# Performance work log

Measured on AMD Instinct MI355X. Metric: run time of the kernel, lower is better.

Reference implementation:

```python
import jax, jax.numpy as jnp
import numpy as np

N_PILLARS_X = 512
N_PILLARS_Y = 512
IN_FEATURES = 6
OUT_FEATURES = 64
N_POINTS = 2_000_000
BN_EPS = 1e-5


def setup_inputs() -> dict:
    key = jax.random.key(0)
    k_x, k_idx, k_w, k_b, k_g, k_bt = jax.random.split(key, 6)
    x = jax.random.normal(k_x, (N_POINTS, IN_FEATURES), dtype=jnp.float32)
    indices = jax.random.randint(k_idx, (N_POINTS, 2), 0, N_PILLARS_X, dtype=jnp.int64)
    # Linear params (torch default init scale ~ 1/sqrt(fan_in))
    bound = 1.0 / np.sqrt(IN_FEATURES)
    W = jax.random.uniform(k_w, (OUT_FEATURES, IN_FEATURES), minval=-bound, maxval=bound, dtype=jnp.float32)
    b = jax.random.uniform(k_b, (OUT_FEATURES,), minval=-bound, maxval=bound, dtype=jnp.float32)
    # BatchNorm affine params (torch init: gamma=1, beta=0; perturb gamma slightly)
    gamma = jnp.ones((OUT_FEATURES,), dtype=jnp.float32)
    beta = jnp.zeros((OUT_FEATURES,), dtype=jnp.float32)
    return {"x": x, "indices": indices, "W": W, "b": b, "gamma": gamma, "beta": beta}


def reference(x, indices, W, b, gamma, beta):
    # Linear: (N, 6) @ (6, 64) + b -> (N, 64)
    h = x @ W.T + b
    # BatchNorm1d (training mode: batch statistics, biased variance)
    mean = jnp.mean(h, axis=0)
    var = jnp.mean(jnp.square(h - mean), axis=0)
    h = gamma * (h - mean) * jax.lax.rsqrt(var + BN_EPS) + beta
    h = jax.nn.relu(h)
    # Scatter-add each point's feature vector into its (x_idx, y_idx) pillar cell
    grid = jnp.zeros((N_PILLARS_X, N_PILLARS_Y, OUT_FEATURES), dtype=h.dtype)
    grid = grid.at[indices[:, 0], indices[:, 1]].add(h)
    return grid
```

## Files before the change

kernel.cpp:

```cpp
#include <hip/hip_runtime.h>
#include <hip/hip_fp16.h>


constexpr int NPTS   = 2000000;
constexpr int NBUCK  = 2048;
constexpr int CPB    = 128;
constexpr int NBLK   = 512;
constexpr int CHUNK  = (NPTS + NBLK - 1) / NBLK;
constexpr float EPS  = 1e-5f;

constexpr int WS_WPH    = 0;
constexpr int WS_BP     = 192;
constexpr int WS_BSTATS = 256;
constexpr int WS_OFFT   = WS_BSTATS + NBLK * 32;
constexpr int WS_REG    = WS_OFFT + (NBUCK + 1) * NBLK / 2;

typedef _Float16 h2v __attribute__((ext_vector_type(2)));

__device__ __forceinline__ float dot2u(unsigned int a, unsigned int b, float c) {
    union { unsigned int u; h2v h; } ca, cb;
    ca.u = a; cb.u = b;
    return __builtin_amdgcn_fdot2(ca.h, cb.h, c, false);
}

__device__ __forceinline__ float wave_sum64(float v) {
#pragma unroll
    for (int off = 32; off > 0; off >>= 1) v += __shfl_down(v, off, 64);
    return v;
}

__global__ __launch_bounds__(1024) void sort_kernel(const float* __restrict__ x,
                                                    const int2* __restrict__ idx,
                                                    unsigned short* __restrict__ offt,
                                                    uint4* __restrict__ regions,
                                                    float* __restrict__ bstats) {
    __shared__ uint4 recs[CHUNK];
    __shared__ int lh[NBUCK];
    __shared__ int wsum[16];
    __shared__ float lstats[16][27];
    const int t = threadIdx.x, lane = t & 63, wv = t >> 6;
    const int blk = blockIdx.x;
    const int ch  = ((blk & 7) << 6) | (blk >> 3);
    const int beg = ch * CHUNK, end = min(NPTS, beg + CHUNK), cnt = end - beg;

    for (int i = t; i < NBUCK; i += 1024) lh[i] = 0;
    __syncthreads();

    for (int p = beg + t; p < end; p += 1024) {
        const int2 ij = idx[p];
        atomicAdd(&lh[(ij.x << 2) | (ij.y >> 7)], 1);
    }
    __syncthreads();

    {
        const int v0 = lh[2 * t], v1 = lh[2 * t + 1];
        const int v = v0 + v1;
        int incl = v;
#pragma unroll
        for (int d = 1; d < 64; d <<= 1) {
            int u = __shfl_up(incl, d, 64);
            if (lane >= d) incl += u;
        }
        if (lane == 63) wsum[wv] = incl;
        __syncthreads();
        int pre = 0;
#pragma unroll
        for (int w = 0; w < 16; ++w) {
            int sv = wsum[w];
            if (w < wv) pre += sv;
        }
        const int excl = pre + incl - v;
        offt[(2 * t) * NBLK + ch]     = (unsigned short)excl;
        offt[(2 * t + 1) * NBLK + ch] = (unsigned short)(excl + v0);
        if (t == 1023) offt[NBUCK * NBLK + ch] = (unsigned short)(excl + v);
        lh[2 * t] = excl;
        lh[2 * t + 1] = excl + v0;
    }
    __syncthreads();

    float acc[27];
#pragma unroll
    for (int i = 0; i < 27; ++i) acc[i] = 0.f;
    for (int p = beg + t; p < end; p += 1024) {
        const int2 ij = idx[p];
        const float2* xp = (const float2*)(x + (size_t)p * 6);
        const float2 a = xp[0], bq = xp[1], cq = xp[2];
        float v[6] = {a.x, a.y, bq.x, bq.y, cq.x, cq.y};
        int c = 6;
#pragma unroll
        for (int k = 0; k < 6; ++k) {
            acc[k] += v[k];
#pragma unroll
            for (int l = k; l < 6; ++l) { acc[c] += v[k] * v[l]; ++c; }
        }
        __half2 h0 = __floats2half2_rn(a.x, a.y);
        __half2 h1 = __floats2half2_rn(bq.x, bq.y);
        __half2 h2 = __floats2half2_rn(cq.x, cq.y);
        const int b = (ij.x << 2) | (ij.y >> 7);
        const int dst = atomicAdd(&lh[b], 1);
        uint4 r;
        r.x = *(const unsigned int*)&h0;
        r.y = *(const unsigned int*)&h1;
        r.z = *(const unsigned int*)&h2;
        r.w = (unsigned int)(ij.y & 127);
        recs[dst] = r;
    }
    __syncthreads();

    uint4* reg = regions + (size_t)ch * CHUNK;
    for (int i = t; i < cnt; i += 1024) reg[i] = recs[i];

#pragma unroll
    for (int i = 0; i < 27; ++i) {
        const float s = wave_sum64(acc[i]);
        if (lane == 0) lstats[wv][i] = s;
    }
    __syncthreads();
    if (t < 32) {
        float s = 0.f;
        if (t < 27)
            for (int w = 0; w < 16; ++w) s += lstats[w][t];
        bstats[ch * 32 + t] = s;
    }
}

__global__ __launch_bounds__(1024) void bnfold_kernel(const float* __restrict__ bstats,
                                                      const float* __restrict__ W,
                                                      const float* __restrict__ b,
                                                      const float* __restrict__ gamma,
                                                      const float* __restrict__ beta,
                                                      float* __restrict__ ws) {
    __shared__ float lred[32][33];
    __shared__ float s27[27];
    __shared__ float m[6], C[36];
    const int t = threadIdx.x;
    {
        const int s = t & 31, seg = t >> 5;
        float a = 0.f;
#pragma unroll 4
        for (int j = 0; j < NBLK / 32; ++j) a += bstats[(seg * (NBLK / 32) + j) * 32 + s];
        lred[seg][s] = a;
    }
    __syncthreads();
    if (t < 27) {
        float s = 0.f;
#pragma unroll
        for (int g = 0; g < 32; ++g) s += lred[g][t];
        s27[t] = s;
    }
    __syncthreads();
    if (t == 0) {
        const float invN = 1.0f / (float)NPTS;
        float mm[6];
        for (int k = 0; k < 6; ++k) { mm[k] = s27[k] * invN; m[k] = mm[k]; }
        int c = 6;
        for (int k = 0; k < 6; ++k)
            for (int l = k; l < 6; ++l) {
                const float cov = s27[c] * invN - mm[k] * mm[l];
                ++c;
                C[k * 6 + l] = cov;
                C[l * 6 + k] = cov;
            }
    }
    __syncthreads();
    if (t < 64) {
        float w[6];
#pragma unroll
        for (int k = 0; k < 6; ++k) w[k] = W[t * 6 + k];
        float mh = b[t];
#pragma unroll
        for (int k = 0; k < 6; ++k) mh += w[k] * m[k];
        float var = 0.f;
#pragma unroll
        for (int k = 0; k < 6; ++k)
#pragma unroll
            for (int l = 0; l < 6; ++l) var += w[k] * w[l] * C[k * 6 + l];
        const float s = gamma[t] * rsqrtf(var + EPS);
        float wp[6];
#pragma unroll
        for (int k = 0; k < 6; ++k) wp[k] = w[k] * s;
        unsigned int* wsu = (unsigned int*)ws;
        __half2 p0 = __floats2half2_rn(wp[0], wp[1]);
        __half2 p1 = __floats2half2_rn(wp[2], wp[3]);
        __half2 p2 = __floats2half2_rn(wp[4], wp[5]);
        wsu[WS_WPH + t * 3 + 0] = *(const unsigned int*)&p0;
        wsu[WS_WPH + t * 3 + 1] = *(const unsigned int*)&p1;
        wsu[WS_WPH + t * 3 + 2] = *(const unsigned int*)&p2;
        ws[WS_BP + t] = beta[t] + s * (b[t] - mh);
    }
}

constexpr int CAP   = 1152;
constexpr int OVCAP = 16;
constexpr int ACCT  = 256;
constexpr int RPT   = (CAP + ACCT - 1) / ACCT;

__global__ __launch_bounds__(ACCT, 8) void accum_kernel(const uint4* __restrict__ regions,
                                                        const unsigned int* __restrict__ offt32,
                                                        const float* __restrict__ wsf,
                                                        float* __restrict__ grid) {
    __shared__ uint4 recs[CAP];
    __shared__ uint4 ovf[OVCAP];
    __shared__ int lhist[CPB];
    __shared__ int cstart[CPB + 1];
    __shared__ int wsum4[4];
    __shared__ int ntot, novf;
    const int t = threadIdx.x, lane = t & 63, wv = t >> 6;
    const int b = ((blockIdx.x & 7) << 8) | (blockIdx.x >> 3);

    for (int i = t; i < CPB; i += ACCT) lhist[i] = 0;
    if (t == 0) novf = 0;

    const unsigned int* wsu = (const unsigned int*)wsf;
    const unsigned int wp0 = wsu[WS_WPH + lane * 3 + 0];
    const unsigned int wp1 = wsu[WS_WPH + lane * 3 + 1];
    const unsigned int wp2 = wsu[WS_WPH + lane * 3 + 2];
    const float bb = wsf[WS_BP + lane];

    const unsigned int A = offt32[b * (NBLK / 2) + t];
    const unsigned int B = offt32[(b + 1) * (NBLK / 2) + t];
    const int o0 = (int)(A & 0xffffu), o1 = (int)(A >> 16);
    const int l0 = (int)(B & 0xffffu) - o0, l1 = (int)(B >> 16) - o1;
    const int tot = l0 + l1;
    int incl = tot;
#pragma unroll
    for (int d = 1; d < 64; d <<= 1) {
        int u = __shfl_up(incl, d, 64);
        if (lane >= d) incl += u;
    }
    if (lane == 63) wsum4[wv] = incl;
    __syncthreads();
    int pre = 0;
#pragma unroll
    for (int w = 0; w < 4; ++w) {
        int sv = wsum4[w];
        if (w < wv) pre += sv;
    }
    const int base0 = pre + incl - tot;
    const int base1 = base0 + l0;
    if (t == ACCT - 1) ntot = base1 + l1;

    {
        const uint4* s0 = regions + (size_t)(2 * t) * CHUNK + o0;
        const uint4* s1 = regions + (size_t)(2 * t + 1) * CHUNK + o1;
        uint4 a0, a1, c0, c1;
        if (l0 > 0) a0 = s0[0];
        if (l1 > 0) c0 = s1[0];
        if (l0 > 1) a1 = s0[1];
        if (l1 > 1) c1 = s1[1];

        auto put = [&](uint4 r, int dst) {
            const int cell = (int)(r.w & 127u);
            const int rk = atomicAdd(&lhist[cell], 1);
            r.w |= (unsigned int)rk << 8;
            if (dst < CAP) recs[dst] = r;
            else { int sl = atomicAdd(&novf, 1); if (sl < OVCAP) ovf[sl] = r; }
        };
        if (l0 > 0) put(a0, base0);
        if (l1 > 0) put(c0, base1);
        if (l0 > 1) put(a1, base0 + 1);
        if (l1 > 1) put(c1, base1 + 1);
        const int kmax = max(l0, l1);
        for (int k = 2; k < kmax; ++k) {
            if (k < l0) put(s0[k], base0 + k);
            if (k < l1) put(s1[k], base1 + k);
        }
    }
    __syncthreads();
    const int nn = min(ntot, CAP);
    const int ovn = min(novf, OVCAP);

    if (wv == 0) {
        const int v0 = lhist[2 * lane], v1 = lhist[2 * lane + 1];
        const int v = v0 + v1;
        int incl2 = v;
#pragma unroll
        for (int d = 1; d < 64; d <<= 1) {
            int u = __shfl_up(incl2, d, 64);
            if (lane >= d) incl2 += u;
        }
        const int excl = incl2 - v;
        cstart[2 * lane] = excl;
        cstart[2 * lane + 1] = excl + v0;
        if (lane == 63) cstart[CPB] = incl2;
    }
    __syncthreads();

    uint4 rv[RPT];
    int dsts[RPT];
#pragma unroll
    for (int u = 0; u < RPT; ++u) {
        const int i = t + u * ACCT;
        dsts[u] = -1;
        if (i < nn) {
            rv[u] = recs[i];
            dsts[u] = cstart[(int)(rv[u].w & 127u)] + (int)(rv[u].w >> 8);
        }
    }
    __syncthreads();

#pragma unroll
    for (int u = 0; u < RPT; ++u)
        if (dsts[u] >= 0) recs[dsts[u]] = rv[u];
    __syncthreads();

    float* gbase = grid + (size_t)b * (CPB * 64);
    for (int c = wv; c < CPB; c += 4) {
        const int cs = __builtin_amdgcn_readfirstlane(cstart[c]);
        const int ce = __builtin_amdgcn_readfirstlane(cstart[c + 1]);
        float acc0 = 0.f, acc1 = 0.f;
        int p = cs;
        for (; p + 1 < ce; p += 2) {
            const uint4 ra = recs[p];
            const uint4 rb = recs[p + 1];
            const float h0 = dot2u(ra.x, wp0, dot2u(ra.y, wp1, dot2u(ra.z, wp2, bb)));
            const float h1 = dot2u(rb.x, wp0, dot2u(rb.y, wp1, dot2u(rb.z, wp2, bb)));
            acc0 += fmaxf(h0, 0.f);
            acc1 += fmaxf(h1, 0.f);
        }
        if (p < ce) {
            const uint4 ra = recs[p];
            acc0 += fmaxf(dot2u(ra.x, wp0, dot2u(ra.y, wp1, dot2u(ra.z, wp2, bb))), 0.f);
        }
        gbase[c * 64 + lane] = acc0 + acc1;
    }

    if (ovn > 0) {
        __syncthreads();
        for (int i = wv; i < ovn; i += 4) {
            const uint4 r = ovf[i];
            const int c = (int)(r.w & 127u);
            const float h = dot2u(r.x, wp0, dot2u(r.y, wp1, dot2u(r.z, wp2, bb)));
            unsafeAtomicAdd(&gbase[c * 64 + lane], fmaxf(h, 0.f));
        }
    }
}

extern "C" void kernel_launch(void* const* d_in, const int* in_sizes, int n_in,
                              void* d_out, int out_size, void* d_ws, size_t ws_size,
                              hipStream_t stream) {
    const float* x       = (const float*)d_in[0];
    const int2*  indices = (const int2*)d_in[1];
    const float* W       = (const float*)d_in[2];
    const float* b       = (const float*)d_in[3];
    const float* gamma   = (const float*)d_in[4];
    const float* beta    = (const float*)d_in[5];
    float* out = (float*)d_out;
    float* wsf = (float*)d_ws;
    int*   wsi = (int*)d_ws;

    unsigned short* offt   = (unsigned short*)(wsi + WS_OFFT);
    unsigned int*   offt32 = (unsigned int*)(wsi + WS_OFFT);
    uint4* regions = (uint4*)(wsi + WS_REG);
    float* bstats  = wsf + WS_BSTATS;

    sort_kernel<<<NBLK, 1024, 0, stream>>>(x, indices, offt, regions, bstats);
    bnfold_kernel<<<1, 1024, 0, stream>>>(bstats, W, b, gamma, beta, wsf);
    accum_kernel<<<NBUCK, ACCT, 0, stream>>>(regions, offt32, wsf, out);
}
```

Before: 192.7 us.

## Split sort into more, smaller blocks to raise occupancy and shrink LDS per block

Doubles the number of sort blocks to 1024 with 512 threads each, halving the per-block chunk so the LDS record buffer shrinks and more blocks fit per CU. The per-block stats scratch now reuses the histogram LDS array. The accum kernel is adapted to gather from four source regions per thread, not two, and records whose final destination overflows the capacity are moved to the overflow list during the reorder. This trades more, smaller source segments per bucket (more scattered reads in accum) for better parallelism in the sort phase.

```diff
diff --git a/kernel.cpp b/kernel.cpp
--- a/kernel.cpp
+++ b/kernel.cpp
@@ -5,7 +5,8 @@
 constexpr int NPTS   = 2000000;
 constexpr int NBUCK  = 2048;
 constexpr int CPB    = 128;
-constexpr int NBLK   = 512;
+constexpr int NBLK   = 1024;
+constexpr int SORT_T = 512;
 constexpr int CHUNK  = (NPTS + NBLK - 1) / NBLK;
 constexpr float EPS  = 1e-5f;
 
@@ -29,33 +30,35 @@
     return v;
 }
 
-__global__ __launch_bounds__(1024) void sort_kernel(const float* __restrict__ x,
-                                                    const int2* __restrict__ idx,
-                                                    unsigned short* __restrict__ offt,
-                                                    uint4* __restrict__ regions,
-                                                    float* __restrict__ bstats) {
+__global__ __launch_bounds__(SORT_T, 8) void sort_kernel(const float* __restrict__ x,
+                                                         const int2* __restrict__ idx,
+                                                         unsigned short* __restrict__ offt,
+                                                         uint4* __restrict__ regions,
+                                                         float* __restrict__ bstats) {
     __shared__ uint4 recs[CHUNK];
     __shared__ int lh[NBUCK];
-    __shared__ int wsum[16];
-    __shared__ float lstats[16][27];
+    __shared__ int wsum[8];
+    float* lstatsf = (float*)lh;
     const int t = threadIdx.x, lane = t & 63, wv = t >> 6;
     const int blk = blockIdx.x;
-    const int ch  = ((blk & 7) << 6) | (blk >> 3);
+    const int ch  = ((blk & 7) << 7) | (blk >> 3);
     const int beg = ch * CHUNK, end = min(NPTS, beg + CHUNK), cnt = end - beg;
 
-    for (int i = t; i < NBUCK; i += 1024) lh[i] = 0;
-    __syncthreads();
-
-    for (int p = beg + t; p < end; p += 1024) {
+    for (int i = t; i < NBUCK; i += SORT_T) lh[i] = 0;
+    __syncthreads();
+
+    for (int p = beg + t; p < end; p += SORT_T) {
         const int2 ij = idx[p];
         atomicAdd(&lh[(ij.x << 2) | (ij.y >> 7)], 1);
     }
     __syncthreads();
 
     {
-        const int v0 = lh[2 * t], v1 = lh[2 * t + 1];
-        const int v = v0 + v1;
-        int incl = v;
+        int v[4];
+#pragma unroll
+        for (int j = 0; j < 4; ++j) v[j] = lh[4 * t + j];
+        const int vs = v[0] + v[1] + v[2] + v[3];
+        int incl = vs;
 #pragma unroll
         for (int d = 1; d < 64; d <<= 1) {
             int u = __shfl_up(incl, d, 64);
@@ -65,23 +68,25 @@
         __syncthreads();
         int pre = 0;
 #pragma unroll
-        for (int w = 0; w < 16; ++w) {
+        for (int w = 0; w < 8; ++w) {
             int sv = wsum[w];
             if (w < wv) pre += sv;
         }
-        const int excl = pre + incl - v;
-        offt[(2 * t) * NBLK + ch]     = (unsigned short)excl;
-        offt[(2 * t + 1) * NBLK + ch] = (unsigned short)(excl + v0);
-        if (t == 1023) offt[NBUCK * NBLK + ch] = (unsigned short)(excl + v);
-        lh[2 * t] = excl;
-        lh[2 * t + 1] = excl + v0;
+        int run = pre + incl - vs;
+#pragma unroll
+        for (int j = 0; j < 4; ++j) {
+            offt[(4 * t + j) * NBLK + ch] = (unsigned short)run;
+            lh[4 * t + j] = run;
+            run += v[j];
+        }
+        if (t == SORT_T - 1) offt[NBUCK * NBLK + ch] = (unsigned short)run;
     }
     __syncthreads();
 
     float acc[27];
 #pragma unroll
     for (int i = 0; i < 27; ++i) acc[i] = 0.f;
-    for (int p = beg + t; p < end; p += 1024) {
+    for (int p = beg + t; p < end; p += SORT_T) {
         const int2 ij = idx[p];
         const float2* xp = (const float2*)(x + (size_t)p * 6);
         const float2 a = xp[0], bq = xp[1], cq = xp[2];
@@ -108,18 +113,18 @@
     __syncthreads();
 
     uint4* reg = regions + (size_t)ch * CHUNK;
-    for (int i = t; i < cnt; i += 1024) reg[i] = recs[i];
+    for (int i = t; i < cnt; i += SORT_T) reg[i] = recs[i];
 
 #pragma unroll
     for (int i = 0; i < 27; ++i) {
         const float s = wave_sum64(acc[i]);
-        if (lane == 0) lstats[wv][i] = s;
+        if (lane == 0) lstatsf[wv * 27 + i] = s;
     }
     __syncthreads();
     if (t < 32) {
         float s = 0.f;
         if (t < 27)
-            for (int w = 0; w < 16; ++w) s += lstats[w][t];
+            for (int w = 0; w < 8; ++w) s += lstatsf[w * 27 + t];
         bstats[ch * 32 + t] = s;
     }
 }
@@ -217,11 +222,16 @@
     const unsigned int wp2 = wsu[WS_WPH + lane * 3 + 2];
     const float bb = wsf[WS_BP + lane];
 
-    const unsigned int A = offt32[b * (NBLK / 2) + t];
-    const unsigned int B = offt32[(b + 1) * (NBLK / 2) + t];
-    const int o0 = (int)(A & 0xffffu), o1 = (int)(A >> 16);
-    const int l0 = (int)(B & 0xffffu) - o0, l1 = (int)(B >> 16) - o1;
-    const int tot = l0 + l1;
+    const unsigned int A0 = offt32[b * (NBLK / 2) + 2 * t];
+    const unsigned int A1 = offt32[b * (NBLK / 2) + 2 * t + 1];
+    const unsigned int B0 = offt32[(b + 1) * (NBLK / 2) + 2 * t];
+    const unsigned int B1 = offt32[(b + 1) * (NBLK / 2) + 2 * t + 1];
+    int o[4], l[4];
+    o[0] = (int)(A0 & 0xffffu); o[1] = (int)(A0 >> 16);
+    o[2] = (int)(A1 & 0xffffu); o[3] = (int)(A1 >> 16);
+    l[0] = (int)(B0 & 0xffffu) - o[0]; l[1] = (int)(B0 >> 16) - o[1];
+    l[2] = (int)(B1 & 0xffffu) - o[2]; l[3] = (int)(B1 >> 16) - o[3];
+    const int tot = l[0] + l[1] + l[2] + l[3];
     int incl = tot;
 #pragma unroll
     for (int d = 1; d < 64; d <<= 1) {
@@ -236,19 +246,18 @@
         int sv = wsum4[w];
         if (w < wv) pre += sv;
     }
-    const int base0 = pre + incl - tot;
-    const int base1 = base0 + l0;
-    if (t == ACCT - 1) ntot = base1 + l1;
+    int base[4];
+    base[0] = pre + incl - tot;
+    base[1] = base[0] + l[0];
+    base[2] = base[1] + l[1];
+    base[3] = base[2] + l[2];
+    if (t == ACCT - 1) ntot = base[3] + l[3];
 
     {
-        const uint4* s0 = regions + (size_t)(2 * t) * CHUNK + o0;
-        const uint4* s1 = regions + (size_t)(2 * t + 1) * CHUNK + o1;
-        uint4 a0, a1, c0, c1;
-        if (l0 > 0) a0 = s0[0];
-        if (l1 > 0) c0 = s1[0];
-        if (l0 > 1) a1 = s0[1];
-        if (l1 > 1) c1 = s1[1];
-
+        const uint4* s[4];
+#pragma unroll
+        for (int j = 0; j < 4; ++j)
+            s[j] = regions + (size_t)(4 * t + j) * CHUNK + o[j];
         auto put = [&](uint4 r, int dst) {
             const int cell = (int)(r.w & 127u);
             const int rk = atomicAdd(&lhist[cell], 1);
@@ -256,19 +265,15 @@
             if (dst < CAP) recs[dst] = r;
             else { int sl = atomicAdd(&novf, 1); if (sl < OVCAP) ovf[sl] = r; }
         };
-        if (l0 > 0) put(a0, base0);
-        if (l1 > 0) put(c0, base1);
-        if (l0 > 1) put(a1, base0 + 1);
-        if (l1 > 1) put(c1, base1 + 1);
-        const int kmax = max(l0, l1);
-        for (int k = 2; k < kmax; ++k) {
-            if (k < l0) put(s0[k], base0 + k);
-            if (k < l1) put(s1[k], base1 + k);
+        const int kmax = max(max(l[0], l[1]), max(l[2], l[3]));
+        for (int k = 0; k < kmax; ++k) {
+#pragma unroll
+            for (int j = 0; j < 4; ++j)
+                if (k < l[j]) put(s[j][k], base[j] + k);
         }
     }
     __syncthreads();
     const int nn = min(ntot, CAP);
-    const int ovn = min(novf, OVCAP);
 
     if (wv == 0) {
         const int v0 = lhist[2 * lane], v1 = lhist[2 * lane + 1];
@@ -295,6 +300,11 @@
         if (i < nn) {
             rv[u] = recs[i];
             dsts[u] = cstart[(int)(rv[u].w & 127u)] + (int)(rv[u].w >> 8);
+            if (dsts[u] >= CAP) {
+                int sl = atomicAdd(&novf, 1);
+                if (sl < OVCAP) ovf[sl] = rv[u];
+                dsts[u] = -1;
+            }
         }
     }
     __syncthreads();
@@ -303,6 +313,7 @@
     for (int u = 0; u < RPT; ++u)
         if (dsts[u] >= 0) recs[dsts[u]] = rv[u];
     __syncthreads();
+    const int ovn = min(novf, OVCAP);
 
     float* gbase = grid + (size_t)b * (CPB * 64);
     for (int c = wv; c < CPB; c += 4) {
@@ -329,9 +340,9 @@
         __syncthreads();
         for (int i = wv; i < ovn; i += 4) {
             const uint4 r = ovf[i];
-            const int c = (int)(r.w & 127u);
+            const int cc = (int)(r.w & 127u);
             const float h = dot2u(r.x, wp0, dot2u(r.y, wp1, dot2u(r.z, wp2, bb)));
-            unsafeAtomicAdd(&gbase[c * 64 + lane], fmaxf(h, 0.f));
+            unsafeAtomicAdd(&gbase[cc * 64 + lane], fmaxf(h, 0.f));
         }
     }
 }
@@ -354,7 +365,7 @@
     uint4* regions = (uint4*)(wsi + WS_REG);
     float* bstats  = wsf + WS_BSTATS;
 
-    sort_kernel<<<NBLK, 1024, 0, stream>>>(x, indices, offt, regions, bstats);
+    sort_kernel<<<NBLK, SORT_T, 0, stream>>>(x, indices, offt, regions, bstats);
     bnfold_kernel<<<1, 1024, 0, stream>>>(bstats, W, b, gamma, beta, wsf);
     accum_kernel<<<NBUCK, ACCT, 0, stream>>>(regions, offt32, wsf, out);
 }
```

After: 198.3 us. +2.9%, slower.

## Drop LDS staging in sort kernel, scatter records directly to global memory

Applied to the files above, without the earlier changes.

The sort kernel no longer stages its whole chunk of records (about 62KB) in shared memory. Each record is written straight to its bucketed slot in the global region, which frees LDS so more blocks can be resident. Block size drops to 512 threads with four buckets per thread in the scan, and the launch bounds allow eight blocks per CU. Because the global scatter is random, the accumulate kernel now also routes records whose in-cell destination exceeds its shared-memory capacity to the overflow path.

```diff
diff --git a/kernel.cpp b/kernel.cpp
--- a/kernel.cpp
+++ b/kernel.cpp
@@ -6,6 +6,7 @@
 constexpr int NBUCK  = 2048;
 constexpr int CPB    = 128;
 constexpr int NBLK   = 512;
+constexpr int SORT_T = 512;
 constexpr int CHUNK  = (NPTS + NBLK - 1) / NBLK;
 constexpr float EPS  = 1e-5f;
 
@@ -29,33 +30,34 @@
     return v;
 }
 
-__global__ __launch_bounds__(1024) void sort_kernel(const float* __restrict__ x,
-                                                    const int2* __restrict__ idx,
-                                                    unsigned short* __restrict__ offt,
-                                                    uint4* __restrict__ regions,
-                                                    float* __restrict__ bstats) {
-    __shared__ uint4 recs[CHUNK];
+__global__ __launch_bounds__(SORT_T, 8) void sort_kernel(const float* __restrict__ x,
+                                                         const int2* __restrict__ idx,
+                                                         unsigned short* __restrict__ offt,
+                                                         uint4* __restrict__ regions,
+                                                         float* __restrict__ bstats) {
     __shared__ int lh[NBUCK];
-    __shared__ int wsum[16];
-    __shared__ float lstats[16][27];
+    __shared__ int wsum[8];
+    __shared__ float lstats[8][27];
     const int t = threadIdx.x, lane = t & 63, wv = t >> 6;
     const int blk = blockIdx.x;
     const int ch  = ((blk & 7) << 6) | (blk >> 3);
-    const int beg = ch * CHUNK, end = min(NPTS, beg + CHUNK), cnt = end - beg;
-
-    for (int i = t; i < NBUCK; i += 1024) lh[i] = 0;
-    __syncthreads();
-
-    for (int p = beg + t; p < end; p += 1024) {
+    const int beg = ch * CHUNK, end = min(NPTS, beg + CHUNK);
+
+    for (int i = t; i < NBUCK; i += SORT_T) lh[i] = 0;
+    __syncthreads();
+
+    for (int p = beg + t; p < end; p += SORT_T) {
         const int2 ij = idx[p];
         atomicAdd(&lh[(ij.x << 2) | (ij.y >> 7)], 1);
     }
     __syncthreads();
 
     {
-        const int v0 = lh[2 * t], v1 = lh[2 * t + 1];
-        const int v = v0 + v1;
-        int incl = v;
+        int v[4];
+#pragma unroll
+        for (int j = 0; j < 4; ++j) v[j] = lh[4 * t + j];
+        const int vs = v[0] + v[1] + v[2] + v[3];
+        int incl = vs;
 #pragma unroll
         for (int d = 1; d < 64; d <<= 1) {
             int u = __shfl_up(incl, d, 64);
@@ -65,23 +67,26 @@
         __syncthreads();
         int pre = 0;
 #pragma unroll
-        for (int w = 0; w < 16; ++w) {
+        for (int w = 0; w < 8; ++w) {
             int sv = wsum[w];
             if (w < wv) pre += sv;
         }
-        const int excl = pre + incl - v;
-        offt[(2 * t) * NBLK + ch]     = (unsigned short)excl;
-        offt[(2 * t + 1) * NBLK + ch] = (unsigned short)(excl + v0);
-        if (t == 1023) offt[NBUCK * NBLK + ch] = (unsigned short)(excl + v);
-        lh[2 * t] = excl;
-        lh[2 * t + 1] = excl + v0;
-    }
-    __syncthreads();
-
+        int run = pre + incl - vs;
+#pragma unroll
+        for (int j = 0; j < 4; ++j) {
+            offt[(4 * t + j) * NBLK + ch] = (unsigned short)run;
+            lh[4 * t + j] = run;
+            run += v[j];
+        }
+        if (t == SORT_T - 1) offt[NBUCK * NBLK + ch] = (unsigned short)run;
+    }
+    __syncthreads();
+
+    uint4* reg = regions + (size_t)ch * CHUNK;
     float acc[27];
 #pragma unroll
     for (int i = 0; i < 27; ++i) acc[i] = 0.f;
-    for (int p = beg + t; p < end; p += 1024) {
+    for (int p = beg + t; p < end; p += SORT_T) {
         const int2 ij = idx[p];
         const float2* xp = (const float2*)(x + (size_t)p * 6);
         const float2 a = xp[0], bq = xp[1], cq = xp[2];
@@ -103,12 +108,8 @@
         r.y = *(const unsigned int*)&h1;
         r.z = *(const unsigned int*)&h2;
         r.w = (unsigned int)(ij.y & 127);
-        recs[dst] = r;
-    }
-    __syncthreads();
-
-    uint4* reg = regions + (size_t)ch * CHUNK;
-    for (int i = t; i < cnt; i += 1024) reg[i] = recs[i];
+        reg[dst] = r;
+    }
 
 #pragma unroll
     for (int i = 0; i < 27; ++i) {
@@ -119,7 +120,7 @@
     if (t < 32) {
         float s = 0.f;
         if (t < 27)
-            for (int w = 0; w < 16; ++w) s += lstats[w][t];
+            for (int w = 0; w < 8; ++w) s += lstats[w][t];
         bstats[ch * 32 + t] = s;
     }
 }
@@ -268,7 +269,6 @@
     }
     __syncthreads();
     const int nn = min(ntot, CAP);
-    const int ovn = min(novf, OVCAP);
 
     if (wv == 0) {
         const int v0 = lhist[2 * lane], v1 = lhist[2 * lane + 1];
@@ -295,6 +295,11 @@
         if (i < nn) {
             rv[u] = recs[i];
             dsts[u] = cstart[(int)(rv[u].w & 127u)] + (int)(rv[u].w >> 8);
+            if (dsts[u] >= CAP) {
+                int sl = atomicAdd(&novf, 1);
+                if (sl < OVCAP) ovf[sl] = rv[u];
+                dsts[u] = -1;
+            }
         }
     }
     __syncthreads();
@@ -303,6 +308,7 @@
     for (int u = 0; u < RPT; ++u)
         if (dsts[u] >= 0) recs[dsts[u]] = rv[u];
     __syncthreads();
+    const int ovn = min(novf, OVCAP);
 
     float* gbase = grid + (size_t)b * (CPB * 64);
     for (int c = wv; c < CPB; c += 4) {
@@ -329,9 +335,9 @@
         __syncthreads();
         for (int i = wv; i < ovn; i += 4) {
             const uint4 r = ovf[i];
-            const int c = (int)(r.w & 127u);
+            const int cc = (int)(r.w & 127u);
             const float h = dot2u(r.x, wp0, dot2u(r.y, wp1, dot2u(r.z, wp2, bb)));
-            unsafeAtomicAdd(&gbase[c * 64 + lane], fmaxf(h, 0.f));
+            unsafeAtomicAdd(&gbase[cc * 64 + lane], fmaxf(h, 0.f));
         }
     }
 }
@@ -354,7 +360,7 @@
     uint4* regions = (uint4*)(wsi + WS_REG);
     float* bstats  = wsf + WS_BSTATS;
 
-    sort_kernel<<<NBLK, 1024, 0, stream>>>(x, indices, offt, regions, bstats);
+    sort_kernel<<<NBLK, SORT_T, 0, stream>>>(x, indices, offt, regions, bstats);
     bnfold_kernel<<<1, 1024, 0, stream>>>(bstats, W, b, gamma, beta, wsf);
     accum_kernel<<<NBUCK, ACCT, 0, stream>>>(regions, offt32, wsf, out);
 }
```

Result: slower. 211.4 us (+9.7%).
